# Optimization experiments

Measured on AMD Instinct MI355X. Metric: run time of the kernel, lower is better.

Reference implementation:

```python
import jax, jax.numpy as jnp
import numpy as np

B, S, C = 2, 4096, 512
H = 8            # num heads
D = C // H       # head dim = 64


def setup_inputs() -> dict:
    key = jax.random.key(0)
    ks = jax.random.split(key, 5)
    s = 0.02
    return {
        "hidden_states": jax.random.normal(ks[0], (B, S, C), dtype=jnp.float32),
        "Wq": jax.random.normal(ks[1], (C, C), dtype=jnp.float32) * s,
        "Wk": jax.random.normal(ks[2], (C, C), dtype=jnp.float32) * s,
        "Wv": jax.random.normal(ks[3], (C, C), dtype=jnp.float32) * s,
        "Wo": jax.random.normal(ks[4], (C, C), dtype=jnp.float32) * s,
        "bo": jnp.zeros((C,), dtype=jnp.float32),
    }


def reference(hidden_states, Wq, Wk, Wv, Wo, bo):
    # Self-attention path of AttnProcessor (encoder_hidden_states=None,
    # no norms, no mask, residual_connection=False, rescale=1.0).
    b, s, c = hidden_states.shape
    scale = jnp.float32(D) ** -0.5
    # QKV projections (Linear, no bias as in diffusers defaults)
    q = hidden_states @ Wq.T   # [b,s,c]
    k = hidden_states @ Wk.T
    v = hidden_states @ Wv.T
    # head_to_batch_dim: [b,s,c] -> [b,s,h,d]
    q = q.reshape(b, s, H, D)
    k = k.reshape(b, s, H, D)
    v = v.reshape(b, s, H, D)
    # get_attention_scores: scaled QK^T + softmax (full O(S^2) matrix, as in source)
    scores = jnp.einsum("bqhd,bkhd->bhqk", q, k) * scale   # [b,h,s,s]
    probs = jax.nn.softmax(scores, axis=-1)
    # bmm with V, batch_to_head_dim
    out = jnp.einsum("bhqk,bkhd->bqhd", probs, v).reshape(b, s, c)
    # to_out[0] (Linear with bias); to_out[1] is Dropout (identity at eval)
    out = out @ Wo.T + bo
    return out
```

## Files before the change

### kernel.cpp

```cpp
#include <hip/hip_runtime.h>
#include <hip/hip_bf16.h>

#define BB 2
#define SS 4096
#define CC 512
#define HH 8
#define DD 64
#define MM (BB*SS)

typedef __bf16 bf16;
typedef __attribute__((ext_vector_type(8))) __bf16 bf16x8;
typedef __attribute__((ext_vector_type(4))) __bf16 bf16x4;
typedef __attribute__((ext_vector_type(4))) float f32x4;

#define LP 72
#define QSCALE 0.18033688f

__device__ __forceinline__ bf16x8 cvt8(const float4 a, const float4 b) {
  bf16x8 r;
  r[0]=(bf16)a.x; r[1]=(bf16)a.y; r[2]=(bf16)a.z; r[3]=(bf16)a.w;
  r[4]=(bf16)b.x; r[5]=(bf16)b.y; r[6]=(bf16)b.z; r[7]=(bf16)b.w;
  return r;
}

__global__ __launch_bounds__(256) void cvt_f32_bf16(
    const float* __restrict__ src, bf16* __restrict__ dst)
{
  size_t e = ((size_t)blockIdx.x * 256 + threadIdx.x) * 8;
  float4 a = ((const float4*)(src + e))[0];
  float4 b = ((const float4*)(src + e))[1];
  *(bf16x8*)(dst + e) = cvt8(a, b);
}

__global__ __launch_bounds__(256) void cvt_w(
    const float* __restrict__ Wq, const float* __restrict__ Wk,
    const float* __restrict__ Wv, bf16* __restrict__ Wb)
{
  size_t e = ((size_t)blockIdx.x * 256 + threadIdx.x) * 8;
  const int tens = (int)(e >> 18);
  const float* src = ((tens == 0) ? Wq : (tens == 1) ? Wk : Wv) + (e & 262143);
  const float sc = (tens == 0) ? QSCALE : 1.f;
  float4 a = ((const float4*)src)[0];
  float4 b = ((const float4*)src)[1];
  bf16x8 r;
  r[0]=(bf16)(a.x*sc); r[1]=(bf16)(a.y*sc); r[2]=(bf16)(a.z*sc); r[3]=(bf16)(a.w*sc);
  r[4]=(bf16)(b.x*sc); r[5]=(bf16)(b.y*sc); r[6]=(bf16)(b.z*sc); r[7]=(bf16)(b.w*sc);
  *(bf16x8*)(Wb + e) = r;
}

__global__ __launch_bounds__(256) void qkv_gemm(
    const bf16* __restrict__ Xb, const bf16* __restrict__ Wb,
    bf16* __restrict__ qp, bf16* __restrict__ kp, bf16* __restrict__ vtp)
{
  __shared__ bf16 Aa[64*LP];
  __shared__ bf16 Ab[64*LP];
  __shared__ bf16 Ba[64*LP];
  __shared__ bf16 Bb[64*LP];
  const int m0  = blockIdx.x * 128;
  const int nf0 = blockIdx.y * 128;
  const int tens = nf0 >> 9;
  const int n0 = nf0 & 511;

  const int t = threadIdx.x;
  const int w = t >> 6;
  const int lane = t & 63;
  const int l15 = lane & 15;
  const int quad = lane >> 4;
  const int srow = t >> 2;
  const int scol = (t & 3) << 4;

  f32x4 acc[2][2][4];
  #pragma unroll
  for (int mi = 0; mi < 2; ++mi)
    #pragma unroll
    for (int ni = 0; ni < 2; ++ni)
      #pragma unroll
      for (int nt = 0; nt < 4; ++nt)
        #pragma unroll
        for (int r = 0; r < 4; ++r) acc[mi][ni][nt][r] = 0.f;

  for (int k0 = 0; k0 < CC; k0 += 64) {
    __syncthreads();
    {
      const bf16* sa = Xb + (size_t)(m0 + srow) * CC + k0 + scol;
      *(bf16x8*)&Aa[srow*LP + scol]     = ((const bf16x8*)sa)[0];
      *(bf16x8*)&Aa[srow*LP + scol + 8] = ((const bf16x8*)sa)[1];
      const bf16* sb = Xb + (size_t)(m0 + 64 + srow) * CC + k0 + scol;
      *(bf16x8*)&Ab[srow*LP + scol]     = ((const bf16x8*)sb)[0];
      *(bf16x8*)&Ab[srow*LP + scol + 8] = ((const bf16x8*)sb)[1];
      const bf16* s1 = Wb + (size_t)(nf0 + srow) * CC + k0 + scol;
      *(bf16x8*)&Ba[srow*LP + scol]     = ((const bf16x8*)s1)[0];
      *(bf16x8*)&Ba[srow*LP + scol + 8] = ((const bf16x8*)s1)[1];
      const bf16* s2 = Wb + (size_t)(nf0 + 64 + srow) * CC + k0 + scol;
      *(bf16x8*)&Bb[srow*LP + scol]     = ((const bf16x8*)s2)[0];
      *(bf16x8*)&Bb[srow*LP + scol + 8] = ((const bf16x8*)s2)[1];
    }
    __syncthreads();
    #pragma unroll
    for (int c = 0; c < 2; ++c) {
      bf16x8 afa = *(const bf16x8*)&Aa[(w*16 + l15)*LP + c*32 + quad*8];
      bf16x8 afb = *(const bf16x8*)&Ab[(w*16 + l15)*LP + c*32 + quad*8];
      #pragma unroll
      for (int nt = 0; nt < 4; ++nt) {
        bf16x8 ba = *(const bf16x8*)&Ba[(nt*16 + l15)*LP + c*32 + quad*8];
        bf16x8 bb = *(const bf16x8*)&Bb[(nt*16 + l15)*LP + c*32 + quad*8];
        acc[0][0][nt] = __builtin_amdgcn_mfma_f32_16x16x32_bf16(afa, ba, acc[0][0][nt], 0, 0, 0);
        acc[1][0][nt] = __builtin_amdgcn_mfma_f32_16x16x32_bf16(afb, ba, acc[1][0][nt], 0, 0, 0);
        acc[0][1][nt] = __builtin_amdgcn_mfma_f32_16x16x32_bf16(afa, bb, acc[0][1][nt], 0, 0, 0);
        acc[1][1][nt] = __builtin_amdgcn_mfma_f32_16x16x32_bf16(afb, bb, acc[1][1][nt], 0, 0, 0);
      }
    }
  }

  bf16* plane = (tens == 0) ? qp : ((tens == 1) ? kp : vtp);
  const int c8 = (t & 7) * 8;

  auto epi = [&](const f32x4* as, int mt0, int nb) {
    const int b = mt0 >> 12, s0g = mt0 & 4095;
    const int h = nb >> 6;
    __syncthreads();
    if (tens < 2) {
      #pragma unroll
      for (int nt = 0; nt < 4; ++nt)
        #pragma unroll
        for (int r = 0; r < 4; ++r)
          Aa[(w*16 + quad*4 + r)*LP + nt*16 + l15] = (bf16)as[nt][r];
    } else {
      #pragma unroll
      for (int nt = 0; nt < 4; ++nt)
        #pragma unroll
        for (int r = 0; r < 4; ++r)
          Aa[(nt*16 + l15)*LP + w*16 + quad*4 + r] = (bf16)as[nt][r];
    }
    __syncthreads();
    #pragma unroll
    for (int i = 0; i < 2; ++i) {
      const int row = (t >> 3) + 32*i;
      bf16x8 v = *(const bf16x8*)&Aa[row*LP + c8];
      if (tens < 2) {
        *(bf16x8*)&plane[((size_t)((b*HH + h)*SS) + s0g + row)*DD + c8] = v;
      } else {
        *(bf16x8*)&plane[((size_t)((b*HH + h)*DD) + row)*SS + s0g + c8] = v;
      }
    }
  };

  epi(acc[0][0], m0,      n0);
  epi(acc[1][0], m0 + 64, n0);
  epi(acc[0][1], m0,      n0 + 64);
  epi(acc[1][1], m0 + 64, n0 + 64);
}

__global__ __launch_bounds__(512, 4) void attn_fa(
    const bf16* __restrict__ qpl, const bf16* __restrict__ kpl,
    const bf16* __restrict__ vtpl, bf16* __restrict__ aout)
{
  __shared__ __align__(16) bf16 smem[2 * 4 * 64 * LP];

  const int t = threadIdx.x;
  const int w = t >> 6;
  const int g = w >> 2;
  const int wl = w & 3;
  const int lane = t & 63;
  const int l15 = lane & 15;
  const int quad = lane >> 4;

  const int lin = blockIdx.x;
  const int bh = lin & 15;
  const int q0 = (lin >> 4) * 128;
  const size_t plane = (size_t)SS * DD;
  const bf16* Qp = qpl + (size_t)bh * plane;
  const bf16* Kp = kpl + (size_t)bh * plane;
  const bf16* Vg = vtpl + (size_t)bh * plane;

  bf16* Ktg = smem + g * (4*64*LP);
  bf16* Vtg = Ktg + 2*64*LP;

  bf16x8 qf[2][2];
  #pragma unroll
  for (int wq = 0; wq < 2; ++wq) {
    const bf16* qr = Qp + (size_t)(q0 + wl*32 + wq*16 + l15) * DD + quad*8;
    qf[wq][0] = *(const bf16x8*)qr;
    qf[wq][1] = *(const bf16x8*)(qr + 32);
  }

  f32x4 o[2][4];
  f32x4 osum[2];
  #pragma unroll
  for (int wq = 0; wq < 2; ++wq) {
    #pragma unroll
    for (int nt = 0; nt < 4; ++nt)
      #pragma unroll
      for (int r = 0; r < 4; ++r) o[wq][nt][r] = 0.f;
    #pragma unroll
    for (int r = 0; r < 4; ++r) osum[wq][r] = 0.f;
  }

  bf16x8 ones;
  #pragma unroll
  for (int i = 0; i < 8; ++i) ones[i] = (bf16)1.0f;

  const int t8  = t & 255;
  const int r0s = t8 >> 2;
  const int cs  = (t8 & 3) << 4;
  const int K0  = ((t8 & 1) << 3) + (((t8 >> 1) & 1) << 5);
  const int kbase = g << 11;

  bf16x8 ka0, ka1, va, vb;
  {
    ka0 = *(const bf16x8*)&Kp[(size_t)(kbase + r0s)*DD + cs];
    ka1 = *(const bf16x8*)&Kp[(size_t)(kbase + r0s)*DD + cs + 8];
    va  = *(const bf16x8*)&Vg[(size_t)r0s*SS + kbase + K0];
    vb  = *(const bf16x8*)&Vg[(size_t)r0s*SS + kbase + K0 + 16];
    *(bf16x8*)&Ktg[r0s*LP + cs]     = ka0;
    *(bf16x8*)&Ktg[r0s*LP + cs + 8] = ka1;
    bf16x8 vv;
    vv[0]=va[0]; vv[1]=va[1]; vv[2]=va[2]; vv[3]=va[3];
    vv[4]=vb[0]; vv[5]=vb[1]; vv[6]=vb[2]; vv[7]=vb[3];
    *(bf16x8*)&Vtg[r0s*LP + cs] = vv;
    vv[0]=va[4]; vv[1]=va[5]; vv[2]=va[6]; vv[3]=va[7];
    vv[4]=vb[4]; vv[5]=vb[5]; vv[6]=vb[6]; vv[7]=vb[7];
    *(bf16x8*)&Vtg[r0s*LP + cs + 8] = vv;
  }
  __syncthreads();

  for (int it = 0; it < 32; ++it) {
    const int cur = it & 1;
    if (it < 31) {
      const int kn = kbase + (it + 1) * 64;
      ka0 = *(const bf16x8*)&Kp[(size_t)(kn + r0s)*DD + cs];
      ka1 = *(const bf16x8*)&Kp[(size_t)(kn + r0s)*DD + cs + 8];
      va  = *(const bf16x8*)&Vg[(size_t)r0s*SS + kn + K0];
      vb  = *(const bf16x8*)&Vg[(size_t)r0s*SS + kn + K0 + 16];
    }

    const bf16* Ktc = Ktg + cur*(64*LP);
    const bf16* Vtc = Vtg + cur*(64*LP);

    f32x4 st[2][4];
    __builtin_amdgcn_s_setprio(1);
    #pragma unroll
    for (int nt = 0; nt < 4; ++nt) {
      bf16x8 kf0 = *(const bf16x8*)&Ktc[(nt*16 + l15)*LP + quad*8];
      bf16x8 kf1 = *(const bf16x8*)&Ktc[(nt*16 + l15)*LP + 32 + quad*8];
      #pragma unroll
      for (int wq = 0; wq < 2; ++wq) {
        f32x4 z; z[0]=z[1]=z[2]=z[3]=0.f;
        z = __builtin_amdgcn_mfma_f32_16x16x32_bf16(kf0, qf[wq][0], z, 0, 0, 0);
        z = __builtin_amdgcn_mfma_f32_16x16x32_bf16(kf1, qf[wq][1], z, 0, 0, 0);
        st[wq][nt] = z;
      }
    }
    __builtin_amdgcn_s_setprio(0);

    bf16x8 pb0[2];
    #pragma unroll
    for (int wq = 0; wq < 2; ++wq)
      #pragma unroll
      for (int nt = 0; nt < 2; ++nt)
        #pragma unroll
        for (int r = 0; r < 4; ++r)
          pb0[wq][(nt & 1)*4 + r] = (bf16)__builtin_amdgcn_exp2f(st[wq][nt][r]);

    __builtin_amdgcn_s_setprio(1);
    #pragma unroll
    for (int nt = 0; nt < 4; ++nt) {
      bf16x8 vf = *(const bf16x8*)&Vtc[(nt*16 + l15)*LP + quad*8];
      #pragma unroll
      for (int wq = 0; wq < 2; ++wq)
        o[wq][nt] = __builtin_amdgcn_mfma_f32_16x16x32_bf16(vf, pb0[wq], o[wq][nt], 0, 0, 0);
    }
    #pragma unroll
    for (int wq = 0; wq < 2; ++wq)
      osum[wq] = __builtin_amdgcn_mfma_f32_16x16x32_bf16(ones, pb0[wq], osum[wq], 0, 0, 0);
    __builtin_amdgcn_s_setprio(0);

    bf16x8 pb1[2];
    #pragma unroll
    for (int wq = 0; wq < 2; ++wq)
      #pragma unroll
      for (int nt = 2; nt < 4; ++nt)
        #pragma unroll
        for (int r = 0; r < 4; ++r)
          pb1[wq][(nt & 1)*4 + r] = (bf16)__builtin_amdgcn_exp2f(st[wq][nt][r]);

    __builtin_amdgcn_s_setprio(1);
    #pragma unroll
    for (int nt = 0; nt < 4; ++nt) {
      bf16x8 vf = *(const bf16x8*)&Vtc[(nt*16 + l15)*LP + 32 + quad*8];
      #pragma unroll
      for (int wq = 0; wq < 2; ++wq)
        o[wq][nt] = __builtin_amdgcn_mfma_f32_16x16x32_bf16(vf, pb1[wq], o[wq][nt], 0, 0, 0);
    }
    #pragma unroll
    for (int wq = 0; wq < 2; ++wq)
      osum[wq] = __builtin_amdgcn_mfma_f32_16x16x32_bf16(ones, pb1[wq], osum[wq], 0, 0, 0);
    __builtin_amdgcn_s_setprio(0);

    if (it < 31) {
      const int nxt = cur ^ 1;
      bf16* Ktn = Ktg + nxt*(64*LP);
      bf16* Vtn = Vtg + nxt*(64*LP);
      *(bf16x8*)&Ktn[r0s*LP + cs]     = ka0;
      *(bf16x8*)&Ktn[r0s*LP + cs + 8] = ka1;
      bf16x8 vv;
      vv[0]=va[0]; vv[1]=va[1]; vv[2]=va[2]; vv[3]=va[3];
      vv[4]=vb[0]; vv[5]=vb[1]; vv[6]=vb[2]; vv[7]=vb[3];
      *(bf16x8*)&Vtn[r0s*LP + cs] = vv;
      vv[0]=va[4]; vv[1]=va[5]; vv[2]=va[6]; vv[3]=va[7];
      vv[4]=vb[4]; vv[5]=vb[5]; vv[6]=vb[6]; vv[7]=vb[7];
      *(bf16x8*)&Vtn[r0s*LP + cs + 8] = vv;
      __syncthreads();
    }
  }

  __syncthreads();
  float* stash = (float*)smem;
  const int sidx = (wl*64 + lane) * 36;
  if (g == 1) {
    #pragma unroll
    for (int wq = 0; wq < 2; ++wq)
      #pragma unroll
      for (int nt = 0; nt < 4; ++nt)
        *(f32x4*)&stash[sidx + (wq*4 + nt)*4] = o[wq][nt];
    stash[sidx + 32] = osum[0][0];
    stash[sidx + 33] = osum[1][0];
  }
  __syncthreads();
  if (g == 0) {
    #pragma unroll
    for (int wq = 0; wq < 2; ++wq)
      #pragma unroll
      for (int nt = 0; nt < 4; ++nt) {
        f32x4 p = *(const f32x4*)&stash[sidx + (wq*4 + nt)*4];
        #pragma unroll
        for (int r = 0; r < 4; ++r) o[wq][nt][r] += p[r];
      }
    const float s0 = osum[0][0] + stash[sidx + 32];
    const float s1 = osum[1][0] + stash[sidx + 33];

    const int b = bh >> 3, h = bh & 7;
    #pragma unroll
    for (int wq = 0; wq < 2; ++wq) {
      const float inv = 1.f / (wq == 0 ? s0 : s1);
      const size_t row = (size_t)(b*SS + q0 + wl*32 + wq*16 + l15) * CC + h*DD;
      #pragma unroll
      for (int nt = 0; nt < 4; ++nt) {
        bf16x4 ov;
        #pragma unroll
        for (int r = 0; r < 4; ++r) ov[r] = (bf16)(o[wq][nt][r] * inv);
        *(bf16x4*)&aout[row + nt*16 + quad*4] = ov;
      }
    }
  }
}

__global__ __launch_bounds__(256) void out_gemm(
    const bf16* __restrict__ A, const bf16* __restrict__ Wob,
    const float* __restrict__ bo, float* __restrict__ out)
{
  __shared__ bf16 Aa[64*LP];
  __shared__ bf16 Ab[64*LP];
  __shared__ bf16 Bt[64*LP];
  const int m0 = blockIdx.x * 128;
  const int n0 = blockIdx.y * 64;

  const int t = threadIdx.x;
  const int w = t >> 6;
  const int lane = t & 63;
  const int l15 = lane & 15;
  const int quad = lane >> 4;
  const int srow = t >> 2;
  const int scol = (t & 3) << 4;

  f32x4 aca[4], acb[4];
  #pragma unroll
  for (int i = 0; i < 4; ++i)
    #pragma unroll
    for (int j = 0; j < 4; ++j) { aca[i][j] = 0.f; acb[i][j] = 0.f; }

  for (int k0 = 0; k0 < CC; k0 += 64) {
    __syncthreads();
    {
      const bf16* sa = A + (size_t)(m0 + srow) * CC + k0 + scol;
      *(bf16x8*)&Aa[srow*LP + scol]     = ((const bf16x8*)sa)[0];
      *(bf16x8*)&Aa[srow*LP + scol + 8] = ((const bf16x8*)sa)[1];
      const bf16* sb = A + (size_t)(m0 + 64 + srow) * CC + k0 + scol;
      *(bf16x8*)&Ab[srow*LP + scol]     = ((const bf16x8*)sb)[0];
      *(bf16x8*)&Ab[srow*LP + scol + 8] = ((const bf16x8*)sb)[1];
      const bf16* s1 = Wob + (size_t)(n0 + srow) * CC + k0 + scol;
      *(bf16x8*)&Bt[srow*LP + scol]     = ((const bf16x8*)s1)[0];
      *(bf16x8*)&Bt[srow*LP + scol + 8] = ((const bf16x8*)s1)[1];
    }
    __syncthreads();
    #pragma unroll
    for (int c = 0; c < 2; ++c) {
      bf16x8 afa = *(const bf16x8*)&Aa[(w*16 + l15)*LP + c*32 + quad*8];
      bf16x8 afb = *(const bf16x8*)&Ab[(w*16 + l15)*LP + c*32 + quad*8];
      #pragma unroll
      for (int nt = 0; nt < 4; ++nt) {
        bf16x8 bfr = *(const bf16x8*)&Bt[(nt*16 + l15)*LP + c*32 + quad*8];
        aca[nt] = __builtin_amdgcn_mfma_f32_16x16x32_bf16(afa, bfr, aca[nt], 0, 0, 0);
        acb[nt] = __builtin_amdgcn_mfma_f32_16x16x32_bf16(afb, bfr, acb[nt], 0, 0, 0);
      }
    }
  }

  #pragma unroll
  for (int nt = 0; nt < 4; ++nt) {
    const int ng = n0 + nt*16 + l15;
    const float bias = bo[ng];
    #pragma unroll
    for (int r = 0; r < 4; ++r) {
      const int mga = m0 + w*16 + quad*4 + r;
      out[(size_t)mga*CC + ng] = aca[nt][r] + bias;
      const int mgb = m0 + 64 + w*16 + quad*4 + r;
      out[(size_t)mgb*CC + ng] = acb[nt][r] + bias;
    }
  }
}

extern "C" void kernel_launch(void* const* d_in, const int* in_sizes, int n_in,
                              void* d_out, int out_size, void* d_ws, size_t ws_size,
                              hipStream_t stream) {
  const float* hs = (const float*)d_in[0];
  const float* Wq = (const float*)d_in[1];
  const float* Wk = (const float*)d_in[2];
  const float* Wv = (const float*)d_in[3];
  const float* Wo = (const float*)d_in[4];
  const float* bo = (const float*)d_in[5];
  float* out = (float*)d_out;

  const size_t PE = (size_t)BB*HH*SS*DD;
  bf16* ws   = (bf16*)d_ws;
  bf16* qp   = ws;
  bf16* kp   = ws + PE;
  bf16* vtp  = ws + 2*PE;
  bf16* Xb   = ws + 3*PE;
  bf16* aout = ws + 3*PE;
  bf16* Wob  = qp;
  bf16* Wb   = ws + 4*PE;

  cvt_f32_bf16<<<dim3(2048),      256, 0, stream>>>(hs, Xb);
  cvt_w       <<<dim3(384),       256, 0, stream>>>(Wq, Wk, Wv, Wb);
  qkv_gemm<<<dim3(MM/128, 12),    256, 0, stream>>>(Xb, Wb, qp, kp, vtp);
  attn_fa <<<dim3(512),           512, 0, stream>>>(qp, kp, vtp, aout);
  cvt_f32_bf16<<<dim3(128),       256, 0, stream>>>(Wo, Wob);
  out_gemm<<<dim3(MM/128, CC/64), 256, 0, stream>>>(aout, Wob, bo, out);
}
```

Baseline: 187.1 us.

## Split QKV GEMM K-loop across two wave groups and fold Wo conversion into cvt_w

The QKV projection kernel now runs 512 threads per block. Two groups of four waves each handle half of the K dimension and are reduced through shared memory before the epilogue, which adds wave-level parallelism to a short K loop. The separate Wo conversion launch is merged into the weight-conversion kernel, with Wob moved into its own workspace slot, which saves one kernel launch. In exchange the GEMM uses more LDS, adds a reduction and extra barriers, and the epilogue now stores with all 512 threads.

Result: slower. 199.1 us (+6.4%).

```diff
diff --git a/kernel.cpp b/kernel.cpp
--- a/kernel.cpp
+++ b/kernel.cpp
@@ -34,28 +34,33 @@
 
 __global__ __launch_bounds__(256) void cvt_w(
     const float* __restrict__ Wq, const float* __restrict__ Wk,
-    const float* __restrict__ Wv, bf16* __restrict__ Wb)
+    const float* __restrict__ Wv, const float* __restrict__ Wo,
+    bf16* __restrict__ Wb, bf16* __restrict__ Wob)
 {
   size_t e = ((size_t)blockIdx.x * 256 + threadIdx.x) * 8;
-  const int tens = (int)(e >> 18);
-  const float* src = ((tens == 0) ? Wq : (tens == 1) ? Wk : Wv) + (e & 262143);
-  const float sc = (tens == 0) ? QSCALE : 1.f;
-  float4 a = ((const float4*)src)[0];
-  float4 b = ((const float4*)src)[1];
-  bf16x8 r;
-  r[0]=(bf16)(a.x*sc); r[1]=(bf16)(a.y*sc); r[2]=(bf16)(a.z*sc); r[3]=(bf16)(a.w*sc);
-  r[4]=(bf16)(b.x*sc); r[5]=(bf16)(b.y*sc); r[6]=(bf16)(b.z*sc); r[7]=(bf16)(b.w*sc);
-  *(bf16x8*)(Wb + e) = r;
-}
-
-__global__ __launch_bounds__(256) void qkv_gemm(
+  if (e < 786432) {
+    const int tens = (int)(e >> 18);
+    const float* src = ((tens == 0) ? Wq : (tens == 1) ? Wk : Wv) + (e & 262143);
+    const float sc = (tens == 0) ? QSCALE : 1.f;
+    float4 a = ((const float4*)src)[0];
+    float4 b = ((const float4*)src)[1];
+    bf16x8 r;
+    r[0]=(bf16)(a.x*sc); r[1]=(bf16)(a.y*sc); r[2]=(bf16)(a.z*sc); r[3]=(bf16)(a.w*sc);
+    r[4]=(bf16)(b.x*sc); r[5]=(bf16)(b.y*sc); r[6]=(bf16)(b.z*sc); r[7]=(bf16)(b.w*sc);
+    *(bf16x8*)(Wb + e) = r;
+  } else {
+    const size_t eo = e - 786432;
+    float4 a = ((const float4*)(Wo + eo))[0];
+    float4 b = ((const float4*)(Wo + eo))[1];
+    *(bf16x8*)(Wob + eo) = cvt8(a, b);
+  }
+}
+
+__global__ __launch_bounds__(512, 4) void qkv_gemm(
     const bf16* __restrict__ Xb, const bf16* __restrict__ Wb,
     bf16* __restrict__ qp, bf16* __restrict__ kp, bf16* __restrict__ vtp)
 {
-  __shared__ bf16 Aa[64*LP];
-  __shared__ bf16 Ab[64*LP];
-  __shared__ bf16 Ba[64*LP];
-  __shared__ bf16 Bb[64*LP];
+  __shared__ __align__(16) bf16 smem[8 * 64 * LP];
   const int m0  = blockIdx.x * 128;
   const int nf0 = blockIdx.y * 128;
   const int tens = nf0 >> 9;
@@ -63,11 +68,20 @@
 
   const int t = threadIdx.x;
   const int w = t >> 6;
+  const int g = w >> 2;
+  const int wl = w & 3;
   const int lane = t & 63;
   const int l15 = lane & 15;
   const int quad = lane >> 4;
-  const int srow = t >> 2;
-  const int scol = (t & 3) << 4;
+  const int t8 = t & 255;
+  const int srow = t8 >> 2;
+  const int scol = (t8 & 3) << 4;
+
+  bf16* Aa = smem + g * (4*64*LP);
+  bf16* Ab = Aa + 64*LP;
+  bf16* Ba = Ab + 64*LP;
+  bf16* Bb = Ba + 64*LP;
+  const int kbase = g << 8;
 
   f32x4 acc[2][2][4];
   #pragma unroll
@@ -79,7 +93,8 @@
         #pragma unroll
         for (int r = 0; r < 4; ++r) acc[mi][ni][nt][r] = 0.f;
 
-  for (int k0 = 0; k0 < CC; k0 += 64) {
+  for (int kk = 0; kk < 4; ++kk) {
+    const int k0 = kbase + kk * 64;
     __syncthreads();
     {
       const bf16* sa = Xb + (size_t)(m0 + srow) * CC + k0 + scol;
@@ -98,8 +113,8 @@
     __syncthreads();
     #pragma unroll
     for (int c = 0; c < 2; ++c) {
-      bf16x8 afa = *(const bf16x8*)&Aa[(w*16 + l15)*LP + c*32 + quad*8];
-      bf16x8 afb = *(const bf16x8*)&Ab[(w*16 + l15)*LP + c*32 + quad*8];
+      bf16x8 afa = *(const bf16x8*)&Aa[(wl*16 + l15)*LP + c*32 + quad*8];
+      bf16x8 afb = *(const bf16x8*)&Ab[(wl*16 + l15)*LP + c*32 + quad*8];
       #pragma unroll
       for (int nt = 0; nt < 4; ++nt) {
         bf16x8 ba = *(const bf16x8*)&Ba[(nt*16 + l15)*LP + c*32 + quad*8];
@@ -112,36 +127,62 @@
     }
   }
 
+  __syncthreads();
+  float* stash = (float*)smem;
+  const int sidx = t8 * 64;
+  if (g == 1) {
+    #pragma unroll
+    for (int mi = 0; mi < 2; ++mi)
+      #pragma unroll
+      for (int ni = 0; ni < 2; ++ni)
+        #pragma unroll
+        for (int nt = 0; nt < 4; ++nt)
+          *(f32x4*)&stash[sidx + ((mi*2 + ni)*4 + nt)*4] = acc[mi][ni][nt];
+  }
+  __syncthreads();
+  if (g == 0) {
+    #pragma unroll
+    for (int mi = 0; mi < 2; ++mi)
+      #pragma unroll
+      for (int ni = 0; ni < 2; ++ni)
+        #pragma unroll
+        for (int nt = 0; nt < 4; ++nt) {
+          f32x4 p = *(const f32x4*)&stash[sidx + ((mi*2 + ni)*4 + nt)*4];
+          #pragma unroll
+          for (int r = 0; r < 4; ++r) acc[mi][ni][nt][r] += p[r];
+        }
+  }
+
   bf16* plane = (tens == 0) ? qp : ((tens == 1) ? kp : vtp);
   const int c8 = (t & 7) * 8;
+  bf16* T = smem;
 
   auto epi = [&](const f32x4* as, int mt0, int nb) {
     const int b = mt0 >> 12, s0g = mt0 & 4095;
     const int h = nb >> 6;
     __syncthreads();
+    if (g == 0) {
+      if (tens < 2) {
+        #pragma unroll
+        for (int nt = 0; nt < 4; ++nt)
+          #pragma unroll
+          for (int r = 0; r < 4; ++r)
+            T[(w*16 + quad*4 + r)*LP + nt*16 + l15] = (bf16)as[nt][r];
+      } else {
+        #pragma unroll
+        for (int nt = 0; nt < 4; ++nt)
+          #pragma unroll
+          for (int r = 0; r < 4; ++r)
+            T[(nt*16 + l15)*LP + w*16 + quad*4 + r] = (bf16)as[nt][r];
+      }
+    }
+    __syncthreads();
+    const int row = t >> 3;
+    bf16x8 v = *(const bf16x8*)&T[row*LP + c8];
     if (tens < 2) {
-      #pragma unroll
-      for (int nt = 0; nt < 4; ++nt)
-        #pragma unroll
-        for (int r = 0; r < 4; ++r)
-          Aa[(w*16 + quad*4 + r)*LP + nt*16 + l15] = (bf16)as[nt][r];
+      *(bf16x8*)&plane[((size_t)((b*HH + h)*SS) + s0g + row)*DD + c8] = v;
     } else {
-      #pragma unroll
-      for (int nt = 0; nt < 4; ++nt)
-        #pragma unroll
-        for (int r = 0; r < 4; ++r)
-          Aa[(nt*16 + l15)*LP + w*16 + quad*4 + r] = (bf16)as[nt][r];
-    }
-    __syncthreads();
-    #pragma unroll
-    for (int i = 0; i < 2; ++i) {
-      const int row = (t >> 3) + 32*i;
-      bf16x8 v = *(const bf16x8*)&Aa[row*LP + c8];
-      if (tens < 2) {
-        *(bf16x8*)&plane[((size_t)((b*HH + h)*SS) + s0g + row)*DD + c8] = v;
-      } else {
-        *(bf16x8*)&plane[((size_t)((b*HH + h)*DD) + row)*SS + s0g + c8] = v;
-      }
+      *(bf16x8*)&plane[((size_t)((b*HH + h)*DD) + row)*SS + s0g + c8] = v;
     }
   };
 
@@ -438,13 +479,12 @@
   bf16* vtp  = ws + 2*PE;
   bf16* Xb   = ws + 3*PE;
   bf16* aout = ws + 3*PE;
-  bf16* Wob  = qp;
   bf16* Wb   = ws + 4*PE;
+  bf16* Wob  = Wb + 786432;
 
   cvt_f32_bf16<<<dim3(2048),      256, 0, stream>>>(hs, Xb);
-  cvt_w       <<<dim3(384),       256, 0, stream>>>(Wq, Wk, Wv, Wb);
-  qkv_gemm<<<dim3(MM/128, 12),    256, 0, stream>>>(Xb, Wb, qp, kp, vtp);
+  cvt_w       <<<dim3(512),       256, 0, stream>>>(Wq, Wk, Wv, Wo, Wb, Wob);
+  qkv_gemm<<<dim3(MM/128, 12),    512, 0, stream>>>(Xb, Wb, qp, kp, vtp);
   attn_fa <<<dim3(512),           512, 0, stream>>>(qp, kp, vtp, aout);
-  cvt_f32_bf16<<<dim3(128),       256, 0, stream>>>(Wo, Wob);
   out_gemm<<<dim3(MM/128, CC/64), 256, 0, stream>>>(aout, Wob, bo, out);
 }
```
